# Optimization experiments

Measured on AMD Instinct MI355X. Metric: run time of the kernel, lower is better.

Reference implementation:

```python
import jax, jax.numpy as jnp
import numpy as np

NUM_HEADS = 16
EPS_LN = 1e-5
EPS_NORM = 1e-12


def layernorm(x, g, b):
    mu = jnp.mean(x, axis=-1, keepdims=True)
    var = jnp.mean((x - mu) ** 2, axis=-1, keepdims=True)
    return (x - mu) * jax.lax.rsqrt(var + EPS_LN) * g + b


def l2norm(x):
    n = jnp.sqrt(jnp.sum(x * x, axis=-1, keepdims=True))
    return x / jnp.maximum(n, EPS_NORM)


def setup_inputs() -> dict:
    key = jax.random.key(0)
    ks = jax.random.split(key, 12)
    B, N, C = 8, 1024, 1024
    std = 0.02
    inp = {
        "txt_token": jax.random.normal(ks[0], (B, 1, C), jnp.float32),
        "text_features": jax.random.normal(ks[1], (B, N, C), jnp.float32),
        "text_mask": jax.random.randint(ks[2], (B, N), 0, 2).astype(bool),
        "vis_token": jax.random.normal(ks[3], (B, 1, C), jnp.float32),
        "top_lens": 256,
        # parameters
        "Wqkv": jax.random.normal(ks[4], (C, 3 * C), jnp.float32) * std,
        "bqkv": jnp.zeros((3 * C,), jnp.float32),
        "Wp2": jax.random.normal(ks[5], (C, C), jnp.float32) * std,
        "bp2": jnp.zeros((C,), jnp.float32),
        "ln2_g": jnp.ones((C,), jnp.float32),
        "ln2_b": jnp.zeros((C,), jnp.float32),
        "sim_alpha": jnp.ones((1,), jnp.float32),
        "sim_beta": jnp.zeros((1,), jnp.float32),
        "Wp1": jax.random.normal(ks[6], (C, C), jnp.float32) * std,
        "bp1": jnp.zeros((C,), jnp.float32),
        "ln1_g": jnp.ones((C,), jnp.float32),
        "ln1_b": jnp.zeros((C,), jnp.float32),
    }
    return inp


def reference(txt_token, text_features, text_mask, vis_token, top_lens,
              Wqkv, bqkv, Wp2, bp2, ln2_g, ln2_b,
              sim_alpha, sim_beta, Wp1, bp1, ln1_g, ln1_b):
    B, N, C = text_features.shape
    H = NUM_HEADS
    hd = C // H
    scale = hd ** (-0.5)

    qkv = (text_features @ Wqkv + bqkv).reshape(B, N, 3, H, hd)
    q = qkv[:, :, 0].transpose(0, 2, 1, 3)  # [B,H,N,hd]
    k = qkv[:, :, 1].transpose(0, 2, 1, 3)
    v = qkv[:, :, 2].transpose(0, 2, 1, 3)

    attn = jnp.einsum('bhqd,bhkd->bhqk', q, k) * scale  # [B,H,N,N]
    vals, idx = jax.lax.top_k(attn, top_lens)            # [B,H,N,k]
    p = jax.nn.softmax(vals, axis=-1)

    # scatter topk softmax back into zeros at original key positions
    b_ix = jnp.arange(B)[:, None, None, None]
    h_ix = jnp.arange(H)[None, :, None, None]
    q_ix = jnp.arange(N)[None, None, :, None]
    attn_sp = jnp.zeros_like(attn).at[b_ix, h_ix, q_ix, idx].set(p)

    # mask padded keys, then second softmax (dropout = identity in eval)
    attn_sp = jnp.where(text_mask[:, None, None, :], -jnp.inf, attn_sp)
    attn_w = jax.nn.softmax(attn_sp, axis=-1)

    x = jnp.einsum('bhqk,bhkd->bqhd', attn_w, v).reshape(B, N, C)
    x = x @ Wp2 + bp2
    tf = layernorm(text_features + x, ln2_g, ln2_b)  # [B,N,C]

    # cosine-similarity top-k pooling
    sim = sim_beta + sim_alpha * jnp.einsum('bmc,bnc->bmn', l2norm(vis_token), l2norm(tf))  # [B,1,N]
    sim = jax.nn.sigmoid(jnp.where(text_mask[:, None, :], -jnp.inf, sim))
    _, top_idx = jax.lax.top_k(sim, top_lens)        # [B,1,k]
    top_idx = top_idx[:, 0]                           # [B,k]
    top_vecs = jnp.take_along_axis(tf, top_idx[:, :, None], axis=1)  # [B,k,C]
    pooled = jnp.mean(top_vecs, axis=1, keepdims=True)               # [B,1,C]

    tt = pooled + txt_token
    tt = layernorm(tt @ Wp1 + bp1, ln1_g, ln1_b)
    return tt, tf
```

## Files before the change

kernel.cpp:

```cpp
#include <hip/hip_runtime.h>
#include <stdint.h>

typedef unsigned short u16;
typedef float floatx4 __attribute__((ext_vector_type(4)));
typedef short short8 __attribute__((ext_vector_type(8)));

#define TOPK_ 256

#define AS1(p) ((const __attribute__((address_space(1))) void*)(p))
#define AS3(p) ((__attribute__((address_space(3))) void*)(p))

__device__ __forceinline__ u16 f2bf(float f) {
  unsigned u = __builtin_bit_cast(unsigned, f);
  unsigned r = (u + 0x7FFFu + ((u >> 16) & 1u)) >> 16;
  return (u16)r;
}
__device__ __forceinline__ float bf2f(u16 b) {
  unsigned u = ((unsigned)b) << 16;
  return __builtin_bit_cast(float, u);
}

__device__ __forceinline__ float wave_sum_f32(float x) {
#define DPP_STEP(ctrl, rmask)                                                        \
  {                                                                                  \
    float t_ = __builtin_bit_cast(                                                   \
        float, __builtin_amdgcn_update_dpp(0, __builtin_bit_cast(int, x), ctrl,      \
                                           rmask, 0xf, true));                       \
    x += t_;                                                                         \
  }
  DPP_STEP(0x111, 0xf)
  DPP_STEP(0x112, 0xf)
  DPP_STEP(0x114, 0xf)
  DPP_STEP(0x118, 0xf)
  DPP_STEP(0x142, 0xa)
  DPP_STEP(0x143, 0xc)
#undef DPP_STEP
  return __builtin_bit_cast(float,
                            __builtin_amdgcn_readlane(__builtin_bit_cast(int, x), 63));
}

__global__ __launch_bounds__(256) void cast_f32_bf16(const float* __restrict__ in,
                                                     u16* __restrict__ out, int n) {
  int i = (blockIdx.x * 256 + threadIdx.x) * 4;
  if (i < n) {
    float4 v = *reinterpret_cast<const float4*>(in + i);
    ushort4 o;
    o.x = f2bf(v.x); o.y = f2bf(v.y); o.z = f2bf(v.z); o.w = f2bf(v.w);
    *reinterpret_cast<ushort4*>(out + i) = o;
  }
}

__global__ __launch_bounds__(256) void transpose_cast(const float* __restrict__ W,
                                                      u16* __restrict__ Wt,
                                                      int rows, int cols) {
  __shared__ u16 tile[32][33];
  int n0 = blockIdx.x * 32, k0 = blockIdx.y * 32;
  int t = threadIdx.x;
  int r = t >> 3, c4 = (t & 7) * 4;
  float4 v = *reinterpret_cast<const float4*>(W + (size_t)(k0 + r) * cols + n0 + c4);
  tile[r][c4 + 0] = f2bf(v.x);
  tile[r][c4 + 1] = f2bf(v.y);
  tile[r][c4 + 2] = f2bf(v.z);
  tile[r][c4 + 3] = f2bf(v.w);
  __syncthreads();
  ushort4 o;
  o.x = tile[c4 + 0][r]; o.y = tile[c4 + 1][r];
  o.z = tile[c4 + 2][r]; o.w = tile[c4 + 3][r];
  *reinterpret_cast<ushort4*>(Wt + (size_t)(n0 + r) * rows + k0 + c4) = o;
}

__global__ __launch_bounds__(256) void gemm_bt(const u16* __restrict__ A,
                                               const u16* __restrict__ Bt,
                                               const float* __restrict__ bias,
                                               int M, int Nn, int K, int mode,
                                               u16* __restrict__ qb, u16* __restrict__ kb,
                                               u16* __restrict__ vb, u16* __restrict__ yb) {
  __shared__ __align__(16) u16 SMEM[9216];
  u16* As = SMEM;
  u16* Bs = SMEM + 4096;
  int id = blockIdx.x + blockIdx.y * gridDim.x;
  int cpx = (gridDim.x * gridDim.y) >> 3;
  int swz = (id & 7) * cpx + (id >> 3);
  int bx = swz % gridDim.x, by = swz / gridDim.x;
  int m0 = by * 128, n0 = bx * 128;
  int t = threadIdx.x, lane = t & 63, wave = t >> 6;
  int wr = wave >> 1, wc = wave & 1;
  int lrow = lane & 15, lko = (lane >> 4) * 8;
  floatx4 acc[4][4];
#pragma unroll
  for (int i = 0; i < 4; ++i)
#pragma unroll
    for (int j = 0; j < 4; ++j) acc[i][j] = (floatx4){0.f, 0.f, 0.f, 0.f};
  int srow = t >> 2, sc8 = (t & 3) * 8;
  const u16* gA0 = A + (size_t)(m0 + srow) * K + sc8;
  const u16* gA1 = A + (size_t)(m0 + srow + 64) * K + sc8;
  const u16* gB0 = Bt + (size_t)(n0 + srow) * K + sc8;
  const u16* gB1 = Bt + (size_t)(n0 + srow + 64) * K + sc8;
  for (int k0 = 0; k0 < K; k0 += 32) {
    __syncthreads();
    __builtin_amdgcn_global_load_lds(AS1(gA0 + k0), AS3(&As[t * 8]), 16, 0, 0);
    __builtin_amdgcn_global_load_lds(AS1(gA1 + k0), AS3(&As[t * 8 + 2048]), 16, 0, 0);
    __builtin_amdgcn_global_load_lds(AS1(gB0 + k0), AS3(&Bs[t * 8]), 16, 0, 0);
    __builtin_amdgcn_global_load_lds(AS1(gB1 + k0), AS3(&Bs[t * 8 + 2048]), 16, 0, 0);
    __syncthreads();
    short8 afr[4], bfr[4];
#pragma unroll
    for (int i = 0; i < 4; ++i) {
      afr[i] = *reinterpret_cast<const short8*>(&As[(wr * 64 + i * 16 + lrow) * 32 + lko]);
      bfr[i] = *reinterpret_cast<const short8*>(&Bs[(wc * 64 + i * 16 + lrow) * 32 + lko]);
    }
#pragma unroll
    for (int i = 0; i < 4; ++i)
#pragma unroll
      for (int j = 0; j < 4; ++j)
        acc[i][j] = __builtin_amdgcn_mfma_f32_16x16x32_bf16(afr[i], bfr[j], acc[i][j], 0, 0, 0);
  }
  int rb = (lane >> 4) * 4;
  if (mode == 0 && n0 >= 2048) {
#pragma unroll
    for (int i = 0; i < 4; ++i) {
#pragma unroll
      for (int j = 0; j < 4; ++j) {
        int gcol = n0 + wc * 64 + j * 16 + lrow;
        float bv = bias[gcol];
        int grow0 = m0 + wr * 64 + i * 16 + rb;
        int cc = gcol & 1023, hh = cc >> 6, dd = cc & 63;
        int bb = grow0 >> 10, nq0 = grow0 & 1023;
        size_t headq = ((size_t)bb * 16 + hh);
        int dtile = dd >> 4, drow = dd & 15;
        int ks32 = nq0 >> 5, kk = nq0 & 31, lq = kk >> 3, e = kk & 7;
        int lane2 = lq * 16 + drow;
        ushort4 o;
        o.x = f2bf(acc[i][j][0] + bv);
        o.y = f2bf(acc[i][j][1] + bv);
        o.z = f2bf(acc[i][j][2] + bv);
        o.w = f2bf(acc[i][j][3] + bv);
        *reinterpret_cast<ushort4*>(vb + headq * 65536 + (size_t)ks32 * 2048 +
                                    dtile * 512 + lane2 * 8 + e) = o;
      }
    }
  } else {
    u16* LDSC = SMEM;
    for (int half = 0; half < 2; ++half) {
      __syncthreads();
      if (wc == half) {
#pragma unroll
        for (int i = 0; i < 4; ++i)
#pragma unroll
          for (int j = 0; j < 4; ++j) {
            float bv = bias[n0 + half * 64 + j * 16 + lrow];
#pragma unroll
            for (int rr = 0; rr < 4; ++rr)
              LDSC[(wr * 64 + i * 16 + rb + rr) * 72 + j * 16 + lrow] =
                  f2bf(acc[i][j][rr] + bv);
          }
      }
      __syncthreads();
      int row = t >> 4, c4 = (t & 15) * 4;
#pragma unroll
      for (int it = 0; it < 8; ++it) {
        int rw = row + it * 16;
        ushort4 val = *reinterpret_cast<const ushort4*>(&LDSC[rw * 72 + c4]);
        int grow = m0 + rw, gcol = n0 + half * 64 + c4;
        if (mode == 1) {
          *reinterpret_cast<ushort4*>(yb + (size_t)grow * 1024 + gcol) = val;
        } else {
          int sec = gcol >> 10, cc = gcol & 1023, hh = cc >> 6, dd = cc & 63;
          int bb = grow >> 10, nq = grow & 1023;
          size_t head = ((size_t)bb * 16 + hh);
          if (sec == 0) {
            *reinterpret_cast<ushort4*>(qb + (head * 1024 + nq) * 64 + dd) = val;
          } else {
            int kc = nq >> 4, krow = nq & 15;
            int p = dd >> 5, quad = (dd >> 3) & 3, e = dd & 7;
            *reinterpret_cast<ushort4*>(kb + head * 65536 + (size_t)kc * 1024 +
                                        p * 512 + (quad * 16 + krow) * 8 + e) = val;
          }
        }
      }
    }
  }
}

#define SSTR 1036
__global__ __launch_bounds__(512, 8) void attn_kernel(const u16* __restrict__ qb,
                                                      const u16* __restrict__ kb,
                                                      const u16* __restrict__ vb,
                                                      const int* __restrict__ mask,
                                                      u16* __restrict__ xout) {
  extern __shared__ __align__(16) char smem[];
  u16* Sb = reinterpret_cast<u16*>(smem);
  u16* qs = reinterpret_cast<u16*>(smem + 33152);
  unsigned char* mk8 = reinterpret_cast<unsigned char*>(smem + 35456);
  float* invZs = reinterpret_cast<float*>(smem + 36480);
  float* part = reinterpret_cast<float*>(smem + 36544);

  int blk = blockIdx.x;
  int bh = blk & 127, qt = blk >> 7;
  int b = bh >> 4, h = bh & 15;
  int t = threadIdx.x, wave = t >> 6, lane = t & 63;
  const u16* qh = qb + ((size_t)bh * 1024 + qt * 16) * 64;
  const u16* kh = kb + (size_t)bh * 65536;
  const u16* vh = vb + (size_t)bh * 65536;

  {
    int2 mm = *reinterpret_cast<const int2*>(mask + b * 1024 + t * 2);
    u16 pk = (u16)((mm.x != 0 ? 1u : 0u) | ((mm.y != 0 ? 1u : 0u) << 8));
    *reinterpret_cast<u16*>(&mk8[t * 2]) = pk;
  }
  if (t < 256) {
    int row = t >> 4, c4 = (t & 15) * 4;
    *reinterpret_cast<ushort4*>(&qs[row * 72 + c4]) =
        *reinterpret_cast<const ushort4*>(qh + row * 64 + c4);
  }
  __syncthreads();

  int lrow = lane & 15, lko = (lane >> 4) * 8;
  int quad = lane >> 4;
  int dtile = wave & 3, kq = wave >> 2;
  const u16* vbase = vh + (size_t)(kq * 16 * 4 + dtile) * 512 + lane * 8;

  {
    short8 qf0 = *reinterpret_cast<const short8*>(&qs[lrow * 72 + lko]);
    short8 qf1 = *reinterpret_cast<const short8*>(&qs[lrow * 72 + lko + 32]);
#pragma unroll 4
    for (int c = 0; c < 8; ++c) {
      int kc = wave * 8 + c;
      const u16* kt = kh + (size_t)kc * 1024 + lane * 8;
      short8 kf0 = *reinterpret_cast<const short8*>(kt);
      short8 kf1 = *reinterpret_cast<const short8*>(kt + 512);
      floatx4 acc = (floatx4){0.f, 0.f, 0.f, 0.f};
      acc = __builtin_amdgcn_mfma_f32_16x16x32_bf16(kf0, qf0, acc, 0, 0, 0);
      acc = __builtin_amdgcn_mfma_f32_16x16x32_bf16(kf1, qf1, acc, 0, 0, 0);
      unsigned kk[4];
#pragma unroll
      for (int i = 0; i < 4; ++i) {
        float f = __builtin_fmaf(acc[i], 64.f, 4096.f);
        f = __builtin_amdgcn_fmed3f(f, 0.f, 8191.f);
        kk[i] = (unsigned)f;
      }
      uint2 pk;
      pk.x = __builtin_amdgcn_perm(kk[1], kk[0], 0x05040100u);
      pk.y = __builtin_amdgcn_perm(kk[3], kk[2], 0x05040100u);
      *reinterpret_cast<uint2*>(&Sb[lrow * SSTR + kc * 16 + quad * 4]) = pk;
    }
  }
  __syncthreads();

  short8 vp0 = *reinterpret_cast<const short8*>(vbase);
  short8 vp1 = *reinterpret_cast<const short8*>(vbase + 2048);
  short8 vp2 = *reinterpret_cast<const short8*>(vbase + 4096);
  short8 vp3 = *reinterpret_cast<const short8*>(vbase + 6144);
  asm volatile("" : "+v"(vp0), "+v"(vp1), "+v"(vp2), "+v"(vp3));

  {
#pragma unroll 1
    for (int rr = 0; rr < 2; ++rr) {
      int row = wave * 2 + rr;
      const u16* Sr = Sb + row * SSTR;
      unsigned k0[16];
#pragma unroll
      for (int jj = 0; jj < 4; ++jj) {
        uint2 p = *reinterpret_cast<const uint2*>(Sr + 4 * lane + 256 * jj);
        k0[4 * jj + 0] = p.x & 0xffffu;
        k0[4 * jj + 1] = p.x >> 16;
        k0[4 * jj + 2] = p.y & 0xffffu;
        k0[4 * jj + 3] = p.y >> 16;
      }
      unsigned T = 0;
      for (int bit = 12; bit >= 5; --bit) {
        unsigned cand = T | (1u << bit);
        int cnt = 0;
#pragma unroll
        for (int i = 0; i < 16; ++i)
          cnt += (int)__popcll(__ballot(k0[i] >= cand));
        if (cnt >= TOPK_) {
          T = cand;
          if (cnt == TOPK_) break;
        }
      }
      const float C1 = 1.44269504f / 512.f;
      const float C0 = -4096.f * (1.44269504f / 512.f);
      float e[16];
      float seq[4] = {0.f, 0.f, 0.f, 0.f};
#pragma unroll
      for (int i = 0; i < 16; ++i) {
        float ex = __builtin_amdgcn_exp2f(__builtin_fmaf((float)k0[i], C1, C0));
        ex = (k0[i] >= T) ? ex : 0.f;
        e[i] = ex;
        seq[i & 3] += ex;
      }
      float se = wave_sum_f32((seq[0] + seq[1]) + (seq[2] + seq[3]));
      float cB = __builtin_amdgcn_rcpf(se) * 1.44269504f;
      float Z = 0.f;
      u16* Wr = Sb + row * SSTR;
#pragma unroll
      for (int jj = 0; jj < 4; ++jj) {
        unsigned m = *reinterpret_cast<const unsigned*>(mk8 + 4 * lane + 256 * jj);
        float w0 = __builtin_amdgcn_exp2f(e[4 * jj + 0] * cB);
        float w1 = __builtin_amdgcn_exp2f(e[4 * jj + 1] * cB);
        float w2 = __builtin_amdgcn_exp2f(e[4 * jj + 2] * cB);
        float w3 = __builtin_amdgcn_exp2f(e[4 * jj + 3] * cB);
        w0 = (m & 0x000000ffu) ? 0.f : w0;
        w1 = (m & 0x0000ff00u) ? 0.f : w1;
        w2 = (m & 0x00ff0000u) ? 0.f : w2;
        w3 = (m & 0xff000000u) ? 0.f : w3;
        Z += (w0 + w1) + (w2 + w3);
        uint2 pw;
        pw.x = __builtin_amdgcn_perm(__builtin_bit_cast(unsigned, w1),
                                     __builtin_bit_cast(unsigned, w0), 0x07060302u);
        pw.y = __builtin_amdgcn_perm(__builtin_bit_cast(unsigned, w3),
                                     __builtin_bit_cast(unsigned, w2), 0x07060302u);
        *reinterpret_cast<uint2*>(Wr + 4 * lane + 256 * jj) = pw;
      }
      Z = wave_sum_f32(Z);
      if (lane == 0) invZs[row] = __builtin_amdgcn_rcpf(Z);
    }
  }
  __syncthreads();

  {
    floatx4 acc = (floatx4){0.f, 0.f, 0.f, 0.f};
    const u16* wrow = Sb + lrow * SSTR + kq * 512;
    short8 af;
    af = *reinterpret_cast<const short8*>(wrow + 0 * 32 + lko);
    acc = __builtin_amdgcn_mfma_f32_16x16x32_bf16(af, vp0, acc, 0, 0, 0);
    af = *reinterpret_cast<const short8*>(wrow + 1 * 32 + lko);
    acc = __builtin_amdgcn_mfma_f32_16x16x32_bf16(af, vp1, acc, 0, 0, 0);
    af = *reinterpret_cast<const short8*>(wrow + 2 * 32 + lko);
    acc = __builtin_amdgcn_mfma_f32_16x16x32_bf16(af, vp2, acc, 0, 0, 0);
    af = *reinterpret_cast<const short8*>(wrow + 3 * 32 + lko);
    acc = __builtin_amdgcn_mfma_f32_16x16x32_bf16(af, vp3, acc, 0, 0, 0);
#pragma unroll
    for (int ks = 4; ks < 16; ++ks) {
      short8 bf = *reinterpret_cast<const short8*>(vbase + (size_t)ks * 2048);
      short8 af2 = *reinterpret_cast<const short8*>(wrow + ks * 32 + lko);
      acc = __builtin_amdgcn_mfma_f32_16x16x32_bf16(af2, bf, acc, 0, 0, 0);
    }
    if (kq == 1)
      *reinterpret_cast<floatx4*>(part + (size_t)(dtile * 64 + lane) * 4) = acc;
    __syncthreads();
    if (kq == 0) {
      floatx4 p2 = *reinterpret_cast<const floatx4*>(part + (size_t)(dtile * 64 + lane) * 4);
      float4 iz = *reinterpret_cast<const float4*>(&invZs[quad * 4]);
      int d = dtile * 16 + lrow;
      u16* xo = xout + ((size_t)(b * 1024 + qt * 16 + quad * 4)) * 1024 + h * 64 + d;
      xo[0 * 1024] = f2bf((acc[0] + p2[0]) * iz.x);
      xo[1 * 1024] = f2bf((acc[1] + p2[1]) * iz.y);
      xo[2 * 1024] = f2bf((acc[2] + p2[2]) * iz.z);
      xo[3 * 1024] = f2bf((acc[3] + p2[3]) * iz.w);
    }
  }
}

__device__ __forceinline__ float block_sum256(float v, volatile float* scratch, int wave,
                                              int lane) {
#pragma unroll
  for (int o = 32; o > 0; o >>= 1) v += __shfl_xor(v, o);
  __syncthreads();
  if (lane == 0) scratch[wave] = v;
  __syncthreads();
  return scratch[0] + scratch[1] + scratch[2] + scratch[3];
}

__global__ __launch_bounds__(256) void vhat_k(const float* __restrict__ vis,
                                              float* __restrict__ vhat) {
  __shared__ float red[4];
  int b = blockIdx.x, t = threadIdx.x, wave = t >> 6, lane = t & 63;
  float4 vv = *reinterpret_cast<const float4*>(vis + b * 1024 + t * 4);
  float sq = vv.x * vv.x + vv.y * vv.y + vv.z * vv.z + vv.w * vv.w;
  sq = block_sum256(sq, red, wave, lane);
  float inv = 1.f / fmaxf(sqrtf(sq), 1e-12f);
  float4 o = make_float4(vv.x * inv, vv.y * inv, vv.z * inv, vv.w * inv);
  *reinterpret_cast<float4*>(vhat + b * 1024 + t * 4) = o;
}

__global__ __launch_bounds__(256) void resid_ln(const u16* __restrict__ y,
                                                const float* __restrict__ text,
                                                const float* __restrict__ g,
                                                const float* __restrict__ be,
                                                const float* __restrict__ vhat,
                                                const int* __restrict__ mask,
                                                const float* __restrict__ alpha,
                                                const float* __restrict__ beta,
                                                float* __restrict__ tf,
                                                float* __restrict__ sim_g) {
  __shared__ float scratch[4];
  int row = blockIdx.x, t = threadIdx.x, wave = t >> 6, lane = t & 63;
  int b = row >> 10;
  ushort4 yv = *reinterpret_cast<const ushort4*>(y + (size_t)row * 1024 + t * 4);
  float4 tv = *reinterpret_cast<const float4*>(text + (size_t)row * 1024 + t * 4);
  float v[4] = {bf2f(yv.x) + tv.x, bf2f(yv.y) + tv.y, bf2f(yv.z) + tv.z, bf2f(yv.w) + tv.w};
  float s = 0.f, sq = 0.f;
#pragma unroll
  for (int j = 0; j < 4; ++j) { s += v[j]; sq += v[j] * v[j]; }
  s = block_sum256(s, scratch, wave, lane);
  sq = block_sum256(sq, scratch, wave, lane);
  float mean = s * (1.f / 1024.f);
  float var = sq * (1.f / 1024.f) - mean * mean;
  float rs = rsqrtf(var + 1e-5f);
  float4 gv = *reinterpret_cast<const float4*>(g + t * 4);
  float4 bv = *reinterpret_cast<const float4*>(be + t * 4);
  float4 hv = *reinterpret_cast<const float4*>(vhat + b * 1024 + t * 4);
  float o[4];
  o[0] = (v[0] - mean) * rs * gv.x + bv.x;
  o[1] = (v[1] - mean) * rs * gv.y + bv.y;
  o[2] = (v[2] - mean) * rs * gv.z + bv.z;
  o[3] = (v[3] - mean) * rs * gv.w + bv.w;
  *reinterpret_cast<float4*>(tf + (size_t)row * 1024 + t * 4) = *reinterpret_cast<float4*>(o);
  float s2 = o[0] * o[0] + o[1] * o[1] + o[2] * o[2] + o[3] * o[3];
  float dd = o[0] * hv.x + o[1] * hv.y + o[2] * hv.z + o[3] * hv.w;
  s2 = block_sum256(s2, scratch, wave, lane);
  dd = block_sum256(dd, scratch, wave, lane);
  if (t == 0) {
    float den = fmaxf(sqrtf(s2), 1e-12f);
    float sv = beta[0] + alpha[0] * dd / den;
    sim_g[row] = mask[row] ? -__builtin_inff() : sv;
  }
}

__global__ __launch_bounds__(256) void topk_pool(const float* __restrict__ sim_g,
                                                 const float* __restrict__ tf,
                                                 float* __restrict__ ttpre_acc) {
  __shared__ int idxl[256];
  __shared__ int scount;
  int b = blockIdx.x, p = blockIdx.y, t = threadIdx.x, lane = t & 63;
  if (t == 0) scount = 0;
  __syncthreads();
  if (t < 64) {
    unsigned uv[16];
#pragma unroll
    for (int j = 0; j < 16; ++j) {
      unsigned x = __builtin_bit_cast(unsigned, sim_g[b * 1024 + lane + 64 * j]);
      uv[j] = (x & 0x80000000u) ? ~x : (x | 0x80000000u);
    }
    unsigned T = 0;
    for (int bit = 31; bit >= 0; --bit) {
      unsigned cand = T | (1u << bit);
      int c = 0;
#pragma unroll
      for (int j = 0; j < 16; ++j) c += __popcll(__ballot(uv[j] >= cand));
      if (c >= TOPK_) {
        T = cand;
        if (c == TOPK_) break;
      }
    }
#pragma unroll
    for (int j = 0; j < 16; ++j) {
      if (uv[j] >= T) {
        int q = atomicAdd(&scount, 1);
        if (q < TOPK_) idxl[q] = lane + 64 * j;
      }
    }
  }
  __syncthreads();
  float4 pa = make_float4(0.f, 0.f, 0.f, 0.f);
  for (int i = p * 64; i < p * 64 + 64; ++i) {
    int n = idxl[i];
    float4 vr = *reinterpret_cast<const float4*>(tf + ((size_t)b * 1024 + n) * 1024 + t * 4);
    pa.x += vr.x; pa.y += vr.y; pa.z += vr.z; pa.w += vr.w;
  }
  atomicAdd(&ttpre_acc[b * 1024 + t * 4 + 0], pa.x);
  atomicAdd(&ttpre_acc[b * 1024 + t * 4 + 1], pa.y);
  atomicAdd(&ttpre_acc[b * 1024 + t * 4 + 2], pa.z);
  atomicAdd(&ttpre_acc[b * 1024 + t * 4 + 3], pa.w);
}

__global__ __launch_bounds__(256) void matvec_p1(const float* __restrict__ ttpre_acc,
                                                 const float* __restrict__ txt,
                                                 const float* __restrict__ Wp1,
                                                 const float* __restrict__ bp1,
                                                 float* __restrict__ ttv) {
  __shared__ float xs[1024];
  __shared__ float red[4][64];
  int b = blockIdx.x, q = blockIdx.y, t = threadIdx.x;
  for (int j = t; j < 1024; j += 256)
    xs[j] = ttpre_acc[b * 1024 + j] * (1.f / 256.f) + txt[b * 1024 + j];
  __syncthreads();
  int r = t >> 6, col = q * 64 + (t & 63);
  float acc = 0.f;
#pragma unroll 8
  for (int c = r * 256; c < r * 256 + 256; ++c) acc += xs[c] * Wp1[(size_t)c * 1024 + col];
  red[r][t & 63] = acc;
  __syncthreads();
  if (t < 64) {
    float o = red[0][t] + red[1][t] + red[2][t] + red[3][t] + bp1[q * 64 + t];
    ttv[b * 1024 + q * 64 + t] = o;
  }
}

__global__ __launch_bounds__(256) void ln_tt(const float* __restrict__ ttv,
                                             const float* __restrict__ g1,
                                             const float* __restrict__ b1,
                                             float* __restrict__ tt_out) {
  __shared__ float red[4];
  int b = blockIdx.x, t = threadIdx.x, wave = t >> 6, lane = t & 63;
  float4 v = *reinterpret_cast<const float4*>(ttv + b * 1024 + t * 4);
  float s = v.x + v.y + v.z + v.w;
  float sq = v.x * v.x + v.y * v.y + v.z * v.z + v.w * v.w;
  s = block_sum256(s, red, wave, lane);
  sq = block_sum256(sq, red, wave, lane);
  float mean = s * (1.f / 1024.f);
  float var = sq * (1.f / 1024.f) - mean * mean;
  float rs = rsqrtf(var + 1e-5f);
  float4 gv = *reinterpret_cast<const float4*>(g1 + t * 4);
  float4 bv = *reinterpret_cast<const float4*>(b1 + t * 4);
  float4 o;
  o.x = (v.x - mean) * rs * gv.x + bv.x;
  o.y = (v.y - mean) * rs * gv.y + bv.y;
  o.z = (v.z - mean) * rs * gv.z + bv.z;
  o.w = (v.w - mean) * rs * gv.w + bv.w;
  *reinterpret_cast<float4*>(tt_out + b * 1024 + t * 4) = o;
}

extern "C" void kernel_launch(void* const* d_in, const int* in_sizes, int n_in, void* d_out,
                              int out_size, void* d_ws, size_t ws_size, hipStream_t stream) {
  (void)in_sizes; (void)n_in; (void)out_size; (void)ws_size;
  const float* txt = (const float*)d_in[0];
  const float* text = (const float*)d_in[1];
  const int* mask = (const int*)d_in[2];
  const float* vis = (const float*)d_in[3];
  const float* Wqkv = (const float*)d_in[5];
  const float* bqkv = (const float*)d_in[6];
  const float* Wp2 = (const float*)d_in[7];
  const float* bp2 = (const float*)d_in[8];
  const float* g2 = (const float*)d_in[9];
  const float* b2 = (const float*)d_in[10];
  const float* alpha = (const float*)d_in[11];
  const float* beta = (const float*)d_in[12];
  const float* Wp1 = (const float*)d_in[13];
  const float* bp1 = (const float*)d_in[14];
  const float* g1 = (const float*)d_in[15];
  const float* b1 = (const float*)d_in[16];

  char* ws = (char*)d_ws;
  const size_t MB = 1u << 20;
  u16* Abf = (u16*)(ws);
  u16* Wtqkv = (u16*)(ws + 16 * MB);
  u16* Wtp2 = (u16*)(ws + 22 * MB);
  u16* qbuf = (u16*)(ws + 24 * MB);
  u16* kbuf = (u16*)(ws + 40 * MB);
  u16* vbuf = (u16*)(ws + 56 * MB);
  u16* ybuf = (u16*)(ws + 72 * MB);
  float* vhat = (float*)(ws + 88 * MB);
  float* sim_g = (float*)(ws + 88 * MB + 65536);
  float* ttpre = (float*)(ws + 88 * MB + 131072);
  float* ttv = (float*)(ws + 88 * MB + 196608);

  float* out = (float*)d_out;
  float* tt_out = out;
  float* tf_out = out + 8 * 1024;

  hipMemsetAsync(ttpre, 0, 8 * 1024 * sizeof(float), stream);
  cast_f32_bf16<<<dim3(8192), dim3(256), 0, stream>>>(text, Abf, 8 * 1024 * 1024);
  transpose_cast<<<dim3(96, 32), dim3(256), 0, stream>>>(Wqkv, Wtqkv, 1024, 3072);
  transpose_cast<<<dim3(32, 32), dim3(256), 0, stream>>>(Wp2, Wtp2, 1024, 1024);
  vhat_k<<<dim3(8), dim3(256), 0, stream>>>(vis, vhat);
  gemm_bt<<<dim3(24, 64), dim3(256), 0, stream>>>(Abf, Wtqkv, bqkv, 8192, 3072, 1024, 0, qbuf,
                                                  kbuf, vbuf, (u16*)nullptr);
  attn_kernel<<<dim3(8192), dim3(512), 40640, stream>>>(qbuf, kbuf, vbuf, mask, Abf);
  gemm_bt<<<dim3(8, 64), dim3(256), 0, stream>>>(Abf, Wtp2, bp2, 8192, 1024, 1024, 1,
                                                 (u16*)nullptr, (u16*)nullptr, (u16*)nullptr,
                                                 ybuf);
  resid_ln<<<dim3(8192), dim3(256), 0, stream>>>(ybuf, text, g2, b2, vhat, mask, alpha, beta,
                                                 tf_out, sim_g);
  topk_pool<<<dim3(8, 4), dim3(256), 0, stream>>>(sim_g, tf_out, ttpre);
  matvec_p1<<<dim3(8, 16), dim3(256), 0, stream>>>(ttpre, txt, Wp1, bp1, ttv);
  ln_tt<<<dim3(8), dim3(256), 0, stream>>>(ttv, g1, b1, tt_out);
}
```

Measured before the change: 473.1 us.

## Merge prep kernels, regroup attention blocks by head, interleave two-row threshold search

Four small preprocessing launches (activation cast, two weight transpose-casts, visual-token normalisation) become one kernel that branches on block index, saving launch overhead. The attention grid now puts consecutive blocks on the same batch-head, so one head's K/V stays hot in L2. The radix threshold search for a wave's two rows now runs both rows together, giving more independent ballots for latency hiding and hoisting the mask loads. The cost is higher register pressure in a kernel launched with an occupancy bound of 8.

```diff
diff --git a/kernel.cpp b/kernel.cpp
--- a/kernel.cpp
+++ b/kernel.cpp
@@ -39,34 +39,61 @@
                             __builtin_amdgcn_readlane(__builtin_bit_cast(int, x), 63));
 }
 
-__global__ __launch_bounds__(256) void cast_f32_bf16(const float* __restrict__ in,
-                                                     u16* __restrict__ out, int n) {
-  int i = (blockIdx.x * 256 + threadIdx.x) * 4;
-  if (i < n) {
-    float4 v = *reinterpret_cast<const float4*>(in + i);
+__device__ __forceinline__ float block_sum256(float v, volatile float* scratch, int wave,
+                                              int lane) {
+#pragma unroll
+  for (int o = 32; o > 0; o >>= 1) v += __shfl_xor(v, o);
+  __syncthreads();
+  if (lane == 0) scratch[wave] = v;
+  __syncthreads();
+  return scratch[0] + scratch[1] + scratch[2] + scratch[3];
+}
+
+__global__ __launch_bounds__(256) void prep_kernel(const float* __restrict__ text,
+                                                   u16* __restrict__ Abf,
+                                                   const float* __restrict__ Wqkv,
+                                                   u16* __restrict__ Wtqkv,
+                                                   const float* __restrict__ Wp2,
+                                                   u16* __restrict__ Wtp2,
+                                                   const float* __restrict__ vis,
+                                                   float* __restrict__ vhat) {
+  __shared__ u16 tile[32][33];
+  __shared__ float red[4];
+  int blk = blockIdx.x, t = threadIdx.x;
+  if (blk < 8192) {
+    int i = (blk * 256 + t) * 4;
+    float4 v = *reinterpret_cast<const float4*>(text + i);
     ushort4 o;
     o.x = f2bf(v.x); o.y = f2bf(v.y); o.z = f2bf(v.z); o.w = f2bf(v.w);
-    *reinterpret_cast<ushort4*>(out + i) = o;
-  }
-}
-
-__global__ __launch_bounds__(256) void transpose_cast(const float* __restrict__ W,
-                                                      u16* __restrict__ Wt,
-                                                      int rows, int cols) {
-  __shared__ u16 tile[32][33];
-  int n0 = blockIdx.x * 32, k0 = blockIdx.y * 32;
-  int t = threadIdx.x;
-  int r = t >> 3, c4 = (t & 7) * 4;
-  float4 v = *reinterpret_cast<const float4*>(W + (size_t)(k0 + r) * cols + n0 + c4);
-  tile[r][c4 + 0] = f2bf(v.x);
-  tile[r][c4 + 1] = f2bf(v.y);
-  tile[r][c4 + 2] = f2bf(v.z);
-  tile[r][c4 + 3] = f2bf(v.w);
-  __syncthreads();
-  ushort4 o;
-  o.x = tile[c4 + 0][r]; o.y = tile[c4 + 1][r];
-  o.z = tile[c4 + 2][r]; o.w = tile[c4 + 3][r];
-  *reinterpret_cast<ushort4*>(Wt + (size_t)(n0 + r) * rows + k0 + c4) = o;
+    *reinterpret_cast<ushort4*>(Abf + i) = o;
+  } else if (blk < 12288) {
+    const float* W;
+    u16* Wt;
+    int cols, id;
+    if (blk < 11264) { W = Wqkv; Wt = Wtqkv; cols = 3072; id = blk - 8192; }
+    else             { W = Wp2;  Wt = Wtp2;  cols = 1024; id = blk - 11264; }
+    int nx = cols >> 5;
+    int n0 = (id % nx) * 32, k0 = (id / nx) * 32;
+    int r = t >> 3, c4 = (t & 7) * 4;
+    float4 v = *reinterpret_cast<const float4*>(W + (size_t)(k0 + r) * cols + n0 + c4);
+    tile[r][c4 + 0] = f2bf(v.x);
+    tile[r][c4 + 1] = f2bf(v.y);
+    tile[r][c4 + 2] = f2bf(v.z);
+    tile[r][c4 + 3] = f2bf(v.w);
+    __syncthreads();
+    ushort4 o;
+    o.x = tile[c4 + 0][r]; o.y = tile[c4 + 1][r];
+    o.z = tile[c4 + 2][r]; o.w = tile[c4 + 3][r];
+    *reinterpret_cast<ushort4*>(Wt + (size_t)(n0 + r) * 1024 + k0 + c4) = o;
+  } else {
+    int b = blk - 12288, wave = t >> 6, lane = t & 63;
+    float4 vv = *reinterpret_cast<const float4*>(vis + b * 1024 + t * 4);
+    float sq = vv.x * vv.x + vv.y * vv.y + vv.z * vv.z + vv.w * vv.w;
+    sq = block_sum256(sq, red, wave, lane);
+    float inv = 1.f / fmaxf(sqrtf(sq), 1e-12f);
+    float4 o = make_float4(vv.x * inv, vv.y * inv, vv.z * inv, vv.w * inv);
+    *reinterpret_cast<float4*>(vhat + b * 1024 + t * 4) = o;
+  }
 }
 
 __global__ __launch_bounds__(256) void gemm_bt(const u16* __restrict__ A,
@@ -196,7 +223,7 @@
   float* part = reinterpret_cast<float*>(smem + 36544);
 
   int blk = blockIdx.x;
-  int bh = blk & 127, qt = blk >> 7;
+  int bh = blk >> 6, qt = blk & 63;
   int b = bh >> 4, h = bh & 15;
   int t = threadIdx.x, wave = t >> 6, lane = t & 63;
   const u16* qh = qb + ((size_t)bh * 1024 + qt * 16) * 64;
@@ -254,53 +281,75 @@
   asm volatile("" : "+v"(vp0), "+v"(vp1), "+v"(vp2), "+v"(vp3));
 
   {
+    const u16* SrA = Sb + (wave * 2) * SSTR;
+    const u16* SrB = Sb + (wave * 2 + 1) * SSTR;
+    unsigned kA[16], kB[16];
+#pragma unroll
+    for (int jj = 0; jj < 4; ++jj) {
+      uint2 pa = *reinterpret_cast<const uint2*>(SrA + 4 * lane + 256 * jj);
+      uint2 pb = *reinterpret_cast<const uint2*>(SrB + 4 * lane + 256 * jj);
+      kA[4 * jj + 0] = pa.x & 0xffffu; kA[4 * jj + 1] = pa.x >> 16;
+      kA[4 * jj + 2] = pa.y & 0xffffu; kA[4 * jj + 3] = pa.y >> 16;
+      kB[4 * jj + 0] = pb.x & 0xffffu; kB[4 * jj + 1] = pb.x >> 16;
+      kB[4 * jj + 2] = pb.y & 0xffffu; kB[4 * jj + 3] = pb.y >> 16;
+    }
+    unsigned TA = 0, TB = 0;
+    int dA = 0, dB = 0;
+    for (int bit = 12; bit >= 5; --bit) {
+      unsigned cA = TA | (1u << bit), cB = TB | (1u << bit);
+      int cntA = 0, cntB = 0;
+#pragma unroll
+      for (int i = 0; i < 16; ++i) {
+        cntA += (int)__popcll(__ballot(kA[i] >= cA));
+        cntB += (int)__popcll(__ballot(kB[i] >= cB));
+      }
+      if (!dA && cntA >= TOPK_) { TA = cA; if (cntA == TOPK_) dA = 1; }
+      if (!dB && cntB >= TOPK_) { TB = cB; if (cntB == TOPK_) dB = 1; }
+      if (dA && dB) break;
+    }
+    unsigned mm[4];
+#pragma unroll
+    for (int jj = 0; jj < 4; ++jj)
+      mm[jj] = *reinterpret_cast<const unsigned*>(mk8 + 4 * lane + 256 * jj);
+    const float C1 = 1.44269504f / 512.f;
+    const float C0 = -4096.f * (1.44269504f / 512.f);
 #pragma unroll 1
     for (int rr = 0; rr < 2; ++rr) {
       int row = wave * 2 + rr;
-      const u16* Sr = Sb + row * SSTR;
-      unsigned k0[16];
-#pragma unroll
-      for (int jj = 0; jj < 4; ++jj) {
-        uint2 p = *reinterpret_cast<const uint2*>(Sr + 4 * lane + 256 * jj);
-        k0[4 * jj + 0] = p.x & 0xffffu;
-        k0[4 * jj + 1] = p.x >> 16;
-        k0[4 * jj + 2] = p.y & 0xffffu;
-        k0[4 * jj + 3] = p.y >> 16;
-      }
-      unsigned T = 0;
-      for (int bit = 12; bit >= 5; --bit) {
-        unsigned cand = T | (1u << bit);
-        int cnt = 0;
-#pragma unroll
-        for (int i = 0; i < 16; ++i)
-          cnt += (int)__popcll(__ballot(k0[i] >= cand));
-        if (cnt >= TOPK_) {
-          T = cand;
-          if (cnt == TOPK_) break;
+      unsigned T = rr ? TB : TA;
+      unsigned kk[16];
+      if (rr == 0) {
+#pragma unroll
+        for (int i = 0; i < 16; ++i) kk[i] = kA[i];
+      } else {
+        const u16* Sr = Sb + row * SSTR;
+#pragma unroll
+        for (int jj = 0; jj < 4; ++jj) {
+          uint2 p = *reinterpret_cast<const uint2*>(Sr + 4 * lane + 256 * jj);
+          kk[4 * jj + 0] = p.x & 0xffffu; kk[4 * jj + 1] = p.x >> 16;
+          kk[4 * jj + 2] = p.y & 0xffffu; kk[4 * jj + 3] = p.y >> 16;
         }
       }
-      const float C1 = 1.44269504f / 512.f;
-      const float C0 = -4096.f * (1.44269504f / 512.f);
       float e[16];
       float seq[4] = {0.f, 0.f, 0.f, 0.f};
 #pragma unroll
       for (int i = 0; i < 16; ++i) {
-        float ex = __builtin_amdgcn_exp2f(__builtin_fmaf((float)k0[i], C1, C0));
-        ex = (k0[i] >= T) ? ex : 0.f;
+        float ex = __builtin_amdgcn_exp2f(__builtin_fmaf((float)kk[i], C1, C0));
+        ex = (kk[i] >= T) ? ex : 0.f;
         e[i] = ex;
         seq[i & 3] += ex;
       }
       float se = wave_sum_f32((seq[0] + seq[1]) + (seq[2] + seq[3]));
-      float cB = __builtin_amdgcn_rcpf(se) * 1.44269504f;
+      float cB2 = __builtin_amdgcn_rcpf(se) * 1.44269504f;
       float Z = 0.f;
       u16* Wr = Sb + row * SSTR;
 #pragma unroll
       for (int jj = 0; jj < 4; ++jj) {
-        unsigned m = *reinterpret_cast<const unsigned*>(mk8 + 4 * lane + 256 * jj);
-        float w0 = __builtin_amdgcn_exp2f(e[4 * jj + 0] * cB);
-        float w1 = __builtin_amdgcn_exp2f(e[4 * jj + 1] * cB);
-        float w2 = __builtin_amdgcn_exp2f(e[4 * jj + 2] * cB);
-        float w3 = __builtin_amdgcn_exp2f(e[4 * jj + 3] * cB);
+        unsigned m = mm[jj];
+        float w0 = __builtin_amdgcn_exp2f(e[4 * jj + 0] * cB2);
+        float w1 = __builtin_amdgcn_exp2f(e[4 * jj + 1] * cB2);
+        float w2 = __builtin_amdgcn_exp2f(e[4 * jj + 2] * cB2);
+        float w3 = __builtin_amdgcn_exp2f(e[4 * jj + 3] * cB2);
         w0 = (m & 0x000000ffu) ? 0.f : w0;
         w1 = (m & 0x0000ff00u) ? 0.f : w1;
         w2 = (m & 0x00ff0000u) ? 0.f : w2;
@@ -351,28 +400,6 @@
       xo[3 * 1024] = f2bf((acc[3] + p2[3]) * iz.w);
     }
   }
-}
-
-__device__ __forceinline__ float block_sum256(float v, volatile float* scratch, int wave,
-                                              int lane) {
-#pragma unroll
-  for (int o = 32; o > 0; o >>= 1) v += __shfl_xor(v, o);
-  __syncthreads();
-  if (lane == 0) scratch[wave] = v;
-  __syncthreads();
-  return scratch[0] + scratch[1] + scratch[2] + scratch[3];
-}
-
-__global__ __launch_bounds__(256) void vhat_k(const float* __restrict__ vis,
-                                              float* __restrict__ vhat) {
-  __shared__ float red[4];
-  int b = blockIdx.x, t = threadIdx.x, wave = t >> 6, lane = t & 63;
-  float4 vv = *reinterpret_cast<const float4*>(vis + b * 1024 + t * 4);
-  float sq = vv.x * vv.x + vv.y * vv.y + vv.z * vv.z + vv.w * vv.w;
-  sq = block_sum256(sq, red, wave, lane);
-  float inv = 1.f / fmaxf(sqrtf(sq), 1e-12f);
-  float4 o = make_float4(vv.x * inv, vv.y * inv, vv.z * inv, vv.w * inv);
-  *reinterpret_cast<float4*>(vhat + b * 1024 + t * 4) = o;
 }
 
 __global__ __launch_bounds__(256) void resid_ln(const u16* __restrict__ y,
@@ -552,10 +579,8 @@
   float* tf_out = out + 8 * 1024;
 
   hipMemsetAsync(ttpre, 0, 8 * 1024 * sizeof(float), stream);
-  cast_f32_bf16<<<dim3(8192), dim3(256), 0, stream>>>(text, Abf, 8 * 1024 * 1024);
-  transpose_cast<<<dim3(96, 32), dim3(256), 0, stream>>>(Wqkv, Wtqkv, 1024, 3072);
-  transpose_cast<<<dim3(32, 32), dim3(256), 0, stream>>>(Wp2, Wtp2, 1024, 1024);
-  vhat_k<<<dim3(8), dim3(256), 0, stream>>>(vis, vhat);
+  prep_kernel<<<dim3(12296), dim3(256), 0, stream>>>(text, Abf, Wqkv, Wtqkv, Wp2, Wtp2, vis,
+                                                     vhat);
   gemm_bt<<<dim3(24, 64), dim3(256), 0, stream>>>(Abf, Wtqkv, bqkv, 8192, 3072, 1024, 0, qbuf,
                                                   kbuf, vbuf, (u16*)nullptr);
   attn_kernel<<<dim3(8192), dim3(512), 40640, stream>>>(qbuf, kbuf, vbuf, mask, Abf);
```

Result: faster. 462.7 us (-2.2%).
